# Performance work log

Measured on AMD Instinct MI355X. Metric: run time of the kernel, lower is better.

## Reference

```python
import jax, jax.numpy as jnp
import numpy as np

B, N, H, IN, OUT = 2, 4096, 64, 32, 8


def setup_inputs() -> dict:
    key = jax.random.key(0)
    ks = jax.random.split(key, 18)
    sc = 0.1  # xavier-ish scale for H=64
    mask = lambda k: (jax.random.uniform(k, (1, N, N)) < 0.1).astype(jnp.float32)
    return {
        "x0": jax.random.normal(ks[0], (B, N, IN), jnp.float32),
        "h0": jax.random.normal(ks[1], (B, N, H), jnp.float32),
        "h1": jax.random.normal(ks[2], (B, N, H), jnp.float32),
        "h2": jax.random.normal(ks[3], (B, N, H), jnp.float32),
        "m00": mask(ks[4]), "m20": mask(ks[5]), "m01": mask(ks[6]),
        "m11": mask(ks[7]), "m12": mask(ks[8]), "m22": mask(ks[9]),
        "Wq": jax.random.normal(ks[10], (3, H, H), jnp.float32) * sc,
        "Wk": jax.random.normal(ks[11], (6, H, H), jnp.float32) * sc,
        "Wsu0": jax.random.normal(ks[12], (H, IN + H), jnp.float32) * sc,
        "Wsu12": jax.random.normal(ks[13], (2, H, H), jnp.float32) * sc,
        "Wdt": jax.random.normal(ks[14], (3, H, H), jnp.float32) * sc,
        "bdt": jnp.zeros((3, H), jnp.float32),
        "step_size": jnp.array(1.0, jnp.float32),
        "out_scale": jnp.array(10.0, jnp.float32),
    }


def _cosine_acc(q, keys_and_masks_and_vals):
    # q: [B,N,H]; each entry: (keys [B,Np,H], mask [1,N,Np], vals [B,Np,H])
    qn = q / jnp.linalg.norm(q, axis=2, keepdims=True)
    acc = 0.0
    for k, m, v in keys_and_masks_and_vals:
        kn = k / jnp.linalg.norm(k, axis=2, keepdims=True)
        scale = 1.0 / jnp.sum(m, axis=2, keepdims=True)
        rel = scale * m * jnp.einsum("bnh,bmh->bnm", qn, kn)  # [B,N,Np]
        acc = acc + jnp.einsum("bnm,bmh->bnh", rel, v)
    return acc


def reference(x0, h0, h1, h2, m00, m20, m01, m11, m12, m22,
              Wq, Wk, Wsu0, Wsu12, Wdt, bdt, step_size, out_scale):
    # queries per successor type, keys per edge; edges (pred->succ):
    # 0->0 (k0), 2->0 (k1), 0->1 (k2), 1->1 (k3), 1->2 (k4), 2->2 (k5)
    q0 = h0 @ Wq[0].T
    q1 = h1 @ Wq[1].T
    q2 = h2 @ Wq[2].T
    acc0 = _cosine_acc(q0, [(h0 @ Wk[0].T, m00, h0), (h2 @ Wk[1].T, m20, h2)])
    acc1 = _cosine_acc(q1, [(h0 @ Wk[2].T, m01, h0), (h1 @ Wk[3].T, m11, h1)])
    acc2 = _cosine_acc(q2, [(h1 @ Wk[4].T, m12, h1), (h2 @ Wk[5].T, m22, h2)])

    def step(h, acc_in, Wsu, t):
        dt = 2.0 * jax.nn.sigmoid(h @ Wdt[t].T + bdt[t]) - 1.0
        return h + step_size * dt * (acc_in @ Wsu.T)

    h0n = step(h0, jnp.concatenate([x0, acc0], axis=2), Wsu0, 0)
    h1n = step(h1, acc1, Wsu12[0], 1)
    h2n = step(h2, acc2, Wsu12[1], 2)
    out2 = out_scale * h2n[:, :, :OUT]
    return (out2, h0n, h1n, h2n)
```

## Files before the change

### kernel.cpp

```cpp
#include <hip/hip_runtime.h>

typedef __bf16 bf16;
typedef bf16 bf16x8 __attribute__((ext_vector_type(8)));
typedef float f32x4 __attribute__((ext_vector_type(4)));
typedef unsigned int uint;
typedef uint u32x4 __attribute__((ext_vector_type(4)));
typedef unsigned short u16x8 __attribute__((ext_vector_type(8)));

constexpr int NT = 4096;

__device__ __forceinline__ bf16x8 ld8f(const float* p) {
    f32x4 a = *(const f32x4*)p;
    f32x4 b = *(const f32x4*)(p + 4);
    bf16x8 v;
    v[0] = (bf16)a[0]; v[1] = (bf16)a[1]; v[2] = (bf16)a[2]; v[3] = (bf16)a[3];
    v[4] = (bf16)b[0]; v[5] = (bf16)b[1]; v[6] = (bf16)b[2]; v[7] = (bf16)b[3];
    return v;
}

__device__ __forceinline__ uint pack2(float a, float b) {
    unsigned short ua = __builtin_bit_cast(unsigned short, (bf16)a);
    unsigned short ub = __builtin_bit_cast(unsigned short, (bf16)b);
    return (uint)ua | ((uint)ub << 16);
}

__global__ __launch_bounds__(256) void prep_kernel(
    const float* __restrict__ h0, const float* __restrict__ h1, const float* __restrict__ h2,
    const float* __restrict__ Wq, const float* __restrict__ Wk,
    bf16* __restrict__ qn, bf16* __restrict__ kn, bf16* __restrict__ vT)
{
    __shared__ __align__(16) unsigned short tlds[4][16][72];
    const int tid = threadIdx.x, wid = tid >> 6, lane = tid & 63;
    const int l15 = lane & 15, quad = lane >> 4;
    const int bx = blockIdx.x;
    const int rt = bx & 127, sl = bx >> 7;
    const int g0 = rt * 64;
    const int grow = g0 + wid * 16 + l15;
    const float* hs[3] = {h0, h1, h2};

    bf16x8 af[3][2];
#pragma unroll
    for (int p = 0; p < 3; p++)
#pragma unroll
        for (int hc = 0; hc < 2; hc++)
            af[p][hc] = ld8f(hs[p] + (size_t)grow * 64 + hc * 32 + quad * 8);

    if (sl == 0) {
        const int gr0 = g0 + wid * 16;
        const int bb = gr0 >> 12, n0 = gr0 & 4095;
#pragma unroll
        for (int p = 0; p < 3; p++) {
#pragma unroll
            for (int hc = 0; hc < 2; hc++)
                *(u16x8*)(&tlds[wid][l15][hc * 32 + quad * 8]) = __builtin_bit_cast(u16x8, af[p][hc]);
            unsigned short vals[16];
#pragma unroll
            for (int r = 0; r < 16; r++) vals[r] = tlds[wid][r][lane];
            uint us[8];
#pragma unroll
            for (int k = 0; k < 8; k++) us[k] = (uint)vals[2 * k] | ((uint)vals[2 * k + 1] << 16);
            uint* dst = (uint*)(vT + ((size_t)(p * 2 + bb) * 64 + lane) * NT + n0);
            u32x4 w0 = {us[0], us[1], us[2], us[3]};
            u32x4 w1 = {us[4], us[5], us[6], us[7]};
            *(u32x4*)dst = w0;
            *(u32x4*)(dst + 4) = w1;
        }
    }

    const int predmap[6] = {0, 2, 0, 1, 1, 2};
    const int pj0 = sl * 3;
#pragma unroll
    for (int pi = 0; pi < 3; pi++) {
        const int pj = pj0 + pi;
        const float* W = (pj < 3) ? (Wq + pj * 4096) : (Wk + (pj - 3) * 4096);
        const int src = (pj < 3) ? pj : predmap[pj - 3];
        bf16* outp = (pj < 3) ? (qn + (size_t)pj * 2 * NT * 64)
                              : (kn + (size_t)(pj - 3) * 2 * NT * 64);
        f32x4 s[4];
#pragma unroll
        for (int it = 0; it < 4; it++) {
            f32x4 acc = {0.f, 0.f, 0.f, 0.f};
#pragma unroll
            for (int hc = 0; hc < 2; hc++) {
                bf16x8 wb = ld8f(W + (size_t)(it * 16 + l15) * 64 + hc * 32 + quad * 8);
                acc = __builtin_amdgcn_mfma_f32_16x16x32_bf16(af[src][hc], wb, acc, 0, 0, 0);
            }
            s[it] = acc;
        }
#pragma unroll
        for (int r = 0; r < 4; r++) {
            float ss = s[0][r] * s[0][r] + s[1][r] * s[1][r] + s[2][r] * s[2][r] + s[3][r] * s[3][r];
            ss += __shfl_xor(ss, 1); ss += __shfl_xor(ss, 2);
            ss += __shfl_xor(ss, 4); ss += __shfl_xor(ss, 8);
            float rn = rsqrtf(ss);
            s[0][r] *= rn; s[1][r] *= rn; s[2][r] *= rn; s[3][r] *= rn;
        }
        const int rowbase = g0 + wid * 16 + quad * 4;
#pragma unroll
        for (int it = 0; it < 4; it++)
#pragma unroll
            for (int r = 0; r < 4; r++)
                outp[(size_t)(rowbase + r) * 64 + it * 16 + l15] = (bf16)s[it][r];
    }
}

template<int JC>
__global__ __launch_bounds__(256, 3) void attn_kernel(
    const bf16* __restrict__ qn, const bf16* __restrict__ kn, const bf16* __restrict__ vT,
    const float* __restrict__ m00, const float* __restrict__ m20, const float* __restrict__ m01,
    const float* __restrict__ m11, const float* __restrict__ m12, const float* __restrict__ m22,
    float* __restrict__ Pacc, float* __restrict__ rsO)
{
    __shared__ __align__(16) bf16 Klds[2][64][72];
    __shared__ __align__(16) bf16 Vlds[2][64][72];
    const int tid = threadIdx.x, wid = tid >> 6, lane = tid & 63;
    const int l15 = lane & 15, quad = lane >> 4;
    const int bx = blockIdx.x;
    const int e = bx / (32 * JC);
    const int rem = bx % (32 * JC);
    const int qt = rem / JC, jcv = rem % JC;
    const int qrow0 = qt * 128, wstrip = wid * 32;
    const int qtypemap[6] = {0, 0, 1, 1, 2, 2};
    const int predmap[6]  = {0, 2, 0, 1, 1, 2};
    const float* masks[6] = {m00, m20, m01, m11, m12, m22};
    const float* __restrict__ mask = masks[e];
    const int qtv = qtypemap[e], pv = predmap[e];
    constexpr int JSPAN = NT / JC;
    constexpr int NI = JSPAN / 64;
    const int jbeg = jcv * JSPAN;

    int s_b[4], s_jl[4], s_ch[4];
#pragma unroll
    for (int i = 0; i < 4; i++) {
        int u = tid + 256 * i;
        s_b[i] = u >> 9; s_jl[i] = (u >> 3) & 63; s_ch[i] = u & 7;
    }

    bf16x8 Qf[2][2][2];
#pragma unroll
    for (int b = 0; b < 2; b++)
#pragma unroll
        for (int mt = 0; mt < 2; mt++)
#pragma unroll
            for (int hc = 0; hc < 2; hc++)
                Qf[b][mt][hc] = *(const bf16x8*)(qn +
                    ((size_t)(qtv * 2 + b) * NT + qrow0 + wstrip + mt * 16 + l15) * 64 +
                    hc * 32 + quad * 8);

    f32x4 acc2[2][4][2];
#pragma unroll
    for (int b = 0; b < 2; b++)
#pragma unroll
        for (int ht = 0; ht < 4; ht++)
#pragma unroll
            for (int mt = 0; mt < 2; mt++) {
                f32x4 z = {0.f, 0.f, 0.f, 0.f};
                acc2[b][ht][mt] = z;
            }
    float rsl[2] = {0.f, 0.f};

    u32x4 kreg[4], vreg[4];
#pragma unroll
    for (int i = 0; i < 4; i++) {
        kreg[i] = *(const u32x4*)(kn + ((size_t)(e * 2 + s_b[i]) * NT + jbeg + s_jl[i]) * 64 + s_ch[i] * 8);
        vreg[i] = *(const u32x4*)(vT + ((size_t)(pv * 2 + s_b[i]) * 64 + s_jl[i]) * NT + jbeg + s_ch[i] * 8);
    }
    f32x4 mv[2][4];
#pragma unroll
    for (int mt = 0; mt < 2; mt++)
#pragma unroll
        for (int jt = 0; jt < 4; jt++)
            mv[mt][jt] = *(const f32x4*)(mask +
                (size_t)(qrow0 + wstrip + mt * 16 + l15) * NT + jbeg + jt * 16 + quad * 4);

#pragma unroll 1
    for (int ji = 0; ji < NI; ji++) {
        const int jn = (ji + 1 < NI) ? (jbeg + (ji + 1) * 64) : jbeg;

        __syncthreads();
#pragma unroll
        for (int i = 0; i < 4; i++) {
            *(u32x4*)(&Klds[s_b[i]][s_jl[i]][s_ch[i] * 8]) = kreg[i];
            *(u32x4*)(&Vlds[s_b[i]][s_jl[i]][s_ch[i] * 8]) = vreg[i];
        }
        __syncthreads();

#pragma unroll
        for (int i = 0; i < 4; i++) {
            kreg[i] = *(const u32x4*)(kn + ((size_t)(e * 2 + s_b[i]) * NT + jn + s_jl[i]) * 64 + s_ch[i] * 8);
            vreg[i] = *(const u32x4*)(vT + ((size_t)(pv * 2 + s_b[i]) * 64 + s_jl[i]) * NT + jn + s_ch[i] * 8);
        }

#pragma unroll
        for (int mt = 0; mt < 2; mt++)
#pragma unroll
            for (int jt = 0; jt < 4; jt++)
                rsl[mt] += mv[mt][jt][0] + mv[mt][jt][1] + mv[mt][jt][2] + mv[mt][jt][3];

        uint Pd[2][4][2][2];
#pragma unroll
        for (int jt = 0; jt < 4; jt++)
#pragma unroll
            for (int b = 0; b < 2; b++)
#pragma unroll
                for (int mt = 0; mt < 2; mt++) {
                    f32x4 sc = {0.f, 0.f, 0.f, 0.f};
#pragma unroll
                    for (int hc = 0; hc < 2; hc++) {
                        bf16x8 a = *(const bf16x8*)(&Klds[b][jt * 16 + l15][hc * 32 + quad * 8]);
                        sc = __builtin_amdgcn_mfma_f32_16x16x32_bf16(a, Qf[b][mt][hc], sc, 0, 0, 0);
                    }
                    sc[0] *= mv[mt][jt][0]; sc[1] *= mv[mt][jt][1];
                    sc[2] *= mv[mt][jt][2]; sc[3] *= mv[mt][jt][3];
                    Pd[b][jt][mt][0] = pack2(sc[0], sc[1]);
                    Pd[b][jt][mt][1] = pack2(sc[2], sc[3]);
                }

#pragma unroll
        for (int mt = 0; mt < 2; mt++)
#pragma unroll
            for (int jt = 0; jt < 4; jt++)
                mv[mt][jt] = *(const f32x4*)(mask +
                    (size_t)(qrow0 + wstrip + mt * 16 + l15) * NT + jn + jt * 16 + quad * 4);

#pragma unroll
        for (int b = 0; b < 2; b++) {
            uint Bf[2][2][4];
#pragma unroll
            for (int mt = 0; mt < 2; mt++)
#pragma unroll
                for (int c = 0; c < 2; c++)
#pragma unroll
                    for (int v = 0; v < 4; v++) {
                        int srclane = ((((quad & 1) * 2 + (v >> 1)) * 16 + l15) << 2);
                        int lo = __builtin_amdgcn_ds_bpermute(srclane, (int)Pd[b][2 * c][mt][v & 1]);
                        int hi = __builtin_amdgcn_ds_bpermute(srclane, (int)Pd[b][2 * c + 1][mt][v & 1]);
                        Bf[mt][c][v] = (quad & 2) ? (uint)hi : (uint)lo;
                    }
#pragma unroll
            for (int ht = 0; ht < 4; ht++)
#pragma unroll
                for (int c = 0; c < 2; c++) {
                    bf16x8 a = *(const bf16x8*)(&Vlds[b][ht * 16 + l15][c * 32 + quad * 8]);
#pragma unroll
                    for (int mt = 0; mt < 2; mt++) {
                        u32x4 t = {Bf[mt][c][0], Bf[mt][c][1], Bf[mt][c][2], Bf[mt][c][3]};
                        bf16x8 bbv = __builtin_bit_cast(bf16x8, t);
                        acc2[b][ht][mt] =
                            __builtin_amdgcn_mfma_f32_16x16x32_bf16(a, bbv, acc2[b][ht][mt], 0, 0, 0);
                    }
                }
        }
    }

#pragma unroll
    for (int b = 0; b < 2; b++)
#pragma unroll
        for (int ht = 0; ht < 4; ht++)
#pragma unroll
            for (int mt = 0; mt < 2; mt++) {
                const int n = qrow0 + wstrip + mt * 16 + l15;
#pragma unroll
                for (int r = 0; r < 4; r++) {
                    const int h = ht * 16 + quad * 4 + r;
                    Pacc[(((size_t)(jcv * 6 + e) * 2 + b) * 64 + h) * NT + n] = acc2[b][ht][mt][r];
                }
            }
#pragma unroll
    for (int mt = 0; mt < 2; mt++) {
        float v = rsl[mt];
        v += __shfl_xor(v, 16);
        v += __shfl_xor(v, 32);
        if (quad == 0)
            rsO[(size_t)(jcv * 6 + e) * NT + qrow0 + wstrip + mt * 16 + l15] = v;
    }
}

template<int JC>
__global__ __launch_bounds__(256) void update_kernel(
    const float* __restrict__ x0, const float* __restrict__ h0,
    const float* __restrict__ h1, const float* __restrict__ h2,
    const float* __restrict__ Wsu0, const float* __restrict__ Wsu12,
    const float* __restrict__ Wdt, const float* __restrict__ bdt,
    const float* __restrict__ stepp, const float* __restrict__ oscp,
    const float* __restrict__ Pacc, const float* __restrict__ rs,
    float* __restrict__ dout)
{
    const int tid = threadIdx.x, wid = tid >> 6, lane = tid & 63;
    const int l15 = lane & 15, quad = lane >> 4;
    const int bx = blockIdx.x;
    const int rt = bx & 127, t = bx >> 7;
    const int g0 = rt * 64;
    const int grow = g0 + wid * 16 + l15;
    const int n = grow & 4095, bb = grow >> 12;
    const float step = *stepp, osc = *oscp;
    const float* hs[3] = {h0, h1, h2};
    const float* __restrict__ ht_base = hs[t];

    bf16x8 afh[2], afacc[2], afx;
#pragma unroll
    for (int hc = 0; hc < 2; hc++)
        afh[hc] = ld8f(ht_base + (size_t)grow * 64 + hc * 32 + quad * 8);
    if (t == 0) afx = ld8f(x0 + (size_t)grow * 32 + quad * 8);

    float s0 = 0.f, s1 = 0.f;
#pragma unroll
    for (int jc = 0; jc < JC; jc++) {
        s0 += rs[(size_t)(jc * 6 + 2 * t) * NT + n];
        s1 += rs[(size_t)(jc * 6 + 2 * t + 1) * NT + n];
    }
    const float i0 = 1.f / s0, i1 = 1.f / s1;
#pragma unroll
    for (int hc = 0; hc < 2; hc++) {
        float S0[8] = {0,0,0,0,0,0,0,0}, S1[8] = {0,0,0,0,0,0,0,0};
#pragma unroll
        for (int jc = 0; jc < JC; jc++) {
            const float* b0 = Pacc + (((size_t)(jc * 6 + 2 * t) * 2 + bb) * 64) * NT + n;
            const float* b1 = Pacc + (((size_t)(jc * 6 + 2 * t + 1) * 2 + bb) * 64) * NT + n;
#pragma unroll
            for (int j = 0; j < 8; j++) {
                const int h = hc * 32 + quad * 8 + j;
                S0[j] += b0[(size_t)h * NT];
                S1[j] += b1[(size_t)h * NT];
            }
        }
        bf16x8 v;
#pragma unroll
        for (int j = 0; j < 8; j++) v[j] = (bf16)(S0[j] * i0 + S1[j] * i1);
        afacc[hc] = v;
    }

    float bdtv[4];
#pragma unroll
    for (int it = 0; it < 4; it++)
        bdtv[it] = bdt[t * 64 + it * 16 + l15];

#pragma unroll
    for (int it = 0; it < 4; it++) {
        f32x4 z = {0.f, 0.f, 0.f, 0.f};
        f32x4 u = {0.f, 0.f, 0.f, 0.f};
#pragma unroll
        for (int hc = 0; hc < 2; hc++) {
            bf16x8 wb = ld8f(Wdt + (size_t)t * 4096 + (size_t)(it * 16 + l15) * 64 + hc * 32 + quad * 8);
            z = __builtin_amdgcn_mfma_f32_16x16x32_bf16(afh[hc], wb, z, 0, 0, 0);
        }
        if (t == 0) {
            bf16x8 w0 = ld8f(Wsu0 + (size_t)(it * 16 + l15) * 96 + quad * 8);
            u = __builtin_amdgcn_mfma_f32_16x16x32_bf16(afx, w0, u, 0, 0, 0);
#pragma unroll
            for (int kc = 0; kc < 2; kc++) {
                bf16x8 wk = ld8f(Wsu0 + (size_t)(it * 16 + l15) * 96 + 32 + kc * 32 + quad * 8);
                u = __builtin_amdgcn_mfma_f32_16x16x32_bf16(afacc[kc], wk, u, 0, 0, 0);
            }
        } else {
#pragma unroll
            for (int kc = 0; kc < 2; kc++) {
                bf16x8 wk = ld8f(Wsu12 + (size_t)(t - 1) * 4096 + (size_t)(it * 16 + l15) * 64 + kc * 32 + quad * 8);
                u = __builtin_amdgcn_mfma_f32_16x16x32_bf16(afacc[kc], wk, u, 0, 0, 0);
            }
        }
        const int colg = it * 16 + l15;
#pragma unroll
        for (int r = 0; r < 4; r++) {
            int row = g0 + wid * 16 + quad * 4 + r;
            float zz = z[r] + bdtv[it];
            float dtv = 2.f / (1.f + __expf(-zz)) - 1.f;
            float hval = ht_base[(size_t)row * 64 + colg];
            float hn = hval + step * dtv * u[r];
            dout[65536 + (size_t)t * 524288 + (size_t)row * 64 + colg] = hn;
            if (t == 2 && colg < 8)
                dout[(size_t)row * 8 + colg] = osc * hn;
        }
    }
}

extern "C" void kernel_launch(void* const* d_in, const int* in_sizes, int n_in,
                              void* d_out, int out_size, void* d_ws, size_t ws_size,
                              hipStream_t stream) {
    const float* x0   = (const float*)d_in[0];
    const float* h0   = (const float*)d_in[1];
    const float* h1   = (const float*)d_in[2];
    const float* h2   = (const float*)d_in[3];
    const float* m00  = (const float*)d_in[4];
    const float* m20  = (const float*)d_in[5];
    const float* m01  = (const float*)d_in[6];
    const float* m11  = (const float*)d_in[7];
    const float* m12  = (const float*)d_in[8];
    const float* m22  = (const float*)d_in[9];
    const float* Wq   = (const float*)d_in[10];
    const float* Wk   = (const float*)d_in[11];
    const float* Wsu0 = (const float*)d_in[12];
    const float* Wsu12= (const float*)d_in[13];
    const float* Wdt  = (const float*)d_in[14];
    const float* bdt  = (const float*)d_in[15];
    const float* step = (const float*)d_in[16];
    const float* oscl = (const float*)d_in[17];

    bf16* qn  = (bf16*)d_ws;
    bf16* kn  = qn + 1572864;
    bf16* vT  = kn + 3145728;
    float* Pacc = (float*)(vT + 1572864);

    auto need = [](size_t jc) { return 12582912 + jc * 12582912 + jc * 98304; };
    const int JC = (ws_size >= need(4)) ? 4 : ((ws_size >= need(2)) ? 2 : 1);

    prep_kernel<<<384, 256, 0, stream>>>(h0, h1, h2, Wq, Wk, qn, kn, vT);

    if (JC == 4) {
        float* rs = Pacc + (size_t)4 * 3145728;
        attn_kernel<4><<<6 * 32 * 4, 256, 0, stream>>>(qn, kn, vT, m00, m20, m01, m11, m12, m22, Pacc, rs);
        update_kernel<4><<<384, 256, 0, stream>>>(x0, h0, h1, h2, Wsu0, Wsu12, Wdt, bdt,
                                                  step, oscl, Pacc, rs, (float*)d_out);
    } else if (JC == 2) {
        float* rs = Pacc + (size_t)2 * 3145728;
        attn_kernel<2><<<6 * 32 * 2, 256, 0, stream>>>(qn, kn, vT, m00, m20, m01, m11, m12, m22, Pacc, rs);
        update_kernel<2><<<384, 256, 0, stream>>>(x0, h0, h1, h2, Wsu0, Wsu12, Wdt, bdt,
                                                  step, oscl, Pacc, rs, (float*)d_out);
    } else {
        float* rs = Pacc + (size_t)1 * 3145728;
        attn_kernel<1><<<6 * 32 * 1, 256, 0, stream>>>(qn, kn, vT, m00, m20, m01, m11, m12, m22, Pacc, rs);
        update_kernel<1><<<384, 256, 0, stream>>>(x0, h0, h1, h2, Wsu0, Wsu12, Wdt, bdt,
                                                  step, oscl, Pacc, rs, (float*)d_out);
    }
}
```

Before: 494.0 us.

## Store split-K partials as packed bf16 and raise key-split count and occupancy

```diff
diff --git a/kernel.cpp b/kernel.cpp
--- a/kernel.cpp
+++ b/kernel.cpp
@@ -23,6 +23,9 @@
     unsigned short ub = __builtin_bit_cast(unsigned short, (bf16)b);
     return (uint)ua | ((uint)ub << 16);
 }
+
+__device__ __forceinline__ float bflo(uint w) { return __builtin_bit_cast(float, w << 16); }
+__device__ __forceinline__ float bfhi(uint w) { return __builtin_bit_cast(float, w & 0xffff0000u); }
 
 __global__ __launch_bounds__(256) void prep_kernel(
     const float* __restrict__ h0, const float* __restrict__ h1, const float* __restrict__ h2,
@@ -105,11 +108,11 @@
 }
 
 template<int JC>
-__global__ __launch_bounds__(256, 3) void attn_kernel(
+__global__ __launch_bounds__(256, 4) void attn_kernel(
     const bf16* __restrict__ qn, const bf16* __restrict__ kn, const bf16* __restrict__ vT,
     const float* __restrict__ m00, const float* __restrict__ m20, const float* __restrict__ m01,
     const float* __restrict__ m11, const float* __restrict__ m12, const float* __restrict__ m22,
-    float* __restrict__ Pacc, float* __restrict__ rsO)
+    uint* __restrict__ Pacc, float* __restrict__ rsO)
 {
     __shared__ __align__(16) bf16 Klds[2][64][72];
     __shared__ __align__(16) bf16 Vlds[2][64][72];
@@ -258,14 +261,14 @@
 #pragma unroll
         for (int ht = 0; ht < 4; ht++)
 #pragma unroll
-            for (int mt = 0; mt < 2; mt++) {
-                const int n = qrow0 + wstrip + mt * 16 + l15;
-#pragma unroll
-                for (int r = 0; r < 4; r++) {
-                    const int h = ht * 16 + quad * 4 + r;
-                    Pacc[(((size_t)(jcv * 6 + e) * 2 + b) * 64 + h) * NT + n] = acc2[b][ht][mt][r];
+            for (int p = 0; p < 2; p++)
+#pragma unroll
+                for (int mt = 0; mt < 2; mt++) {
+                    const int n = qrow0 + wstrip + mt * 16 + l15;
+                    const int h2 = ht * 8 + quad * 2 + p;
+                    Pacc[(((size_t)(jcv * 6 + e) * 2 + b) * 32 + h2) * NT + n] =
+                        pack2(acc2[b][ht][mt][2 * p], acc2[b][ht][mt][2 * p + 1]);
                 }
-            }
 #pragma unroll
     for (int mt = 0; mt < 2; mt++) {
         float v = rsl[mt];
@@ -283,7 +286,7 @@
     const float* __restrict__ Wsu0, const float* __restrict__ Wsu12,
     const float* __restrict__ Wdt, const float* __restrict__ bdt,
     const float* __restrict__ stepp, const float* __restrict__ oscp,
-    const float* __restrict__ Pacc, const float* __restrict__ rs,
+    const uint* __restrict__ Pacc, const float* __restrict__ rs,
     float* __restrict__ dout)
 {
     const int tid = threadIdx.x, wid = tid >> 6, lane = tid & 63;
@@ -315,13 +318,17 @@
         float S0[8] = {0,0,0,0,0,0,0,0}, S1[8] = {0,0,0,0,0,0,0,0};
 #pragma unroll
         for (int jc = 0; jc < JC; jc++) {
-            const float* b0 = Pacc + (((size_t)(jc * 6 + 2 * t) * 2 + bb) * 64) * NT + n;
-            const float* b1 = Pacc + (((size_t)(jc * 6 + 2 * t + 1) * 2 + bb) * 64) * NT + n;
-#pragma unroll
-            for (int j = 0; j < 8; j++) {
-                const int h = hc * 32 + quad * 8 + j;
-                S0[j] += b0[(size_t)h * NT];
-                S1[j] += b1[(size_t)h * NT];
+            const uint* b0 = Pacc + (((size_t)(jc * 6 + 2 * t) * 2 + bb) * 32) * NT + n;
+            const uint* b1 = Pacc + (((size_t)(jc * 6 + 2 * t + 1) * 2 + bb) * 32) * NT + n;
+#pragma unroll
+            for (int jp = 0; jp < 4; jp++) {
+                const int h2 = hc * 16 + quad * 4 + jp;
+                uint w0 = b0[(size_t)h2 * NT];
+                uint w1 = b1[(size_t)h2 * NT];
+                S0[2 * jp]     += bflo(w0);
+                S0[2 * jp + 1] += bfhi(w0);
+                S1[2 * jp]     += bflo(w1);
+                S1[2 * jp + 1] += bfhi(w1);
             }
         }
         bf16x8 v;
@@ -399,27 +406,27 @@
     bf16* qn  = (bf16*)d_ws;
     bf16* kn  = qn + 1572864;
     bf16* vT  = kn + 3145728;
-    float* Pacc = (float*)(vT + 1572864);
-
-    auto need = [](size_t jc) { return 12582912 + jc * 12582912 + jc * 98304; };
-    const int JC = (ws_size >= need(4)) ? 4 : ((ws_size >= need(2)) ? 2 : 1);
+    uint* Pacc = (uint*)(vT + 1572864);
+
+    auto need = [](size_t jc) { return 12582912 + jc * 6291456 + jc * 98304; };
+    const int JC = (ws_size >= need(8)) ? 8 : ((ws_size >= need(4)) ? 4 : 2);
 
     prep_kernel<<<384, 256, 0, stream>>>(h0, h1, h2, Wq, Wk, qn, kn, vT);
 
-    if (JC == 4) {
-        float* rs = Pacc + (size_t)4 * 3145728;
+    if (JC == 8) {
+        float* rs = (float*)(Pacc + (size_t)8 * 1572864);
+        attn_kernel<8><<<6 * 32 * 8, 256, 0, stream>>>(qn, kn, vT, m00, m20, m01, m11, m12, m22, Pacc, rs);
+        update_kernel<8><<<384, 256, 0, stream>>>(x0, h0, h1, h2, Wsu0, Wsu12, Wdt, bdt,
+                                                  step, oscl, Pacc, rs, (float*)d_out);
+    } else if (JC == 4) {
+        float* rs = (float*)(Pacc + (size_t)4 * 1572864);
         attn_kernel<4><<<6 * 32 * 4, 256, 0, stream>>>(qn, kn, vT, m00, m20, m01, m11, m12, m22, Pacc, rs);
         update_kernel<4><<<384, 256, 0, stream>>>(x0, h0, h1, h2, Wsu0, Wsu12, Wdt, bdt,
                                                   step, oscl, Pacc, rs, (float*)d_out);
-    } else if (JC == 2) {
-        float* rs = Pacc + (size_t)2 * 3145728;
+    } else {
+        float* rs = (float*)(Pacc + (size_t)2 * 1572864);
         attn_kernel<2><<<6 * 32 * 2, 256, 0, stream>>>(qn, kn, vT, m00, m20, m01, m11, m12, m22, Pacc, rs);
         update_kernel<2><<<384, 256, 0, stream>>>(x0, h0, h1, h2, Wsu0, Wsu12, Wdt, bdt,
                                                   step, oscl, Pacc, rs, (float*)d_out);
-    } else {
-        float* rs = Pacc + (size_t)1 * 3145728;
-        attn_kernel<1><<<6 * 32 * 1, 256, 0, stream>>>(qn, kn, vT, m00, m20, m01, m11, m12, m22, Pacc, rs);
-        update_kernel<1><<<384, 256, 0, stream>>>(x0, h0, h1, h2, Wsu0, Wsu12, Wdt, bdt,
-                                                  step, oscl, Pacc, rs, (float*)d_out);
-    }
-}
+    }
+}
```

Result: slower. 664.8 us (+34.6%).
